# Performance work log

Hardware: AMD Instinct MI355X
Metric: run time of the kernel (lower is better)

Reference implementation:

```python
import jax, jax.numpy as jnp
import numpy as np

DIST_THRESHOLD = 0.1  # distance_threshold from __init__
NO_CODE_ID = -1


def setup_inputs() -> dict:
    key = jax.random.key(0)
    k1, k2 = jax.random.split(key)
    x = jax.random.normal(k1, (16, 4096, 64), dtype=jnp.float32)
    codes = jax.random.normal(k2, (4096, 64), dtype=jnp.float32)  # active codebook rows
    return {"x": x, "codes": codes}


def reference(x, codes):
    # Squared Euclidean distance (cdist ** 2) via the expansion
    x2 = jnp.sum(x * x, axis=-1, keepdims=True)            # [B, N, 1]
    c2 = jnp.sum(codes * codes, axis=-1)                    # [M]
    d2 = x2 + c2 - 2.0 * jnp.einsum("bnd,md->bnm", x, codes)  # [B, N, M]
    within = jnp.any(d2 <= DIST_THRESHOLD, axis=-1)         # [B, N]
    nn_ids = jnp.argmin(d2, axis=-1)                        # [B, N]
    return jnp.where(within, nn_ids, NO_CODE_ID)
```

## Files before the change

### kernel.cpp

```cpp
#include <hip/hip_runtime.h>
#include <stdint.h>

typedef float f32x4 __attribute__((ext_vector_type(4)));
typedef __bf16 bf16x8 __attribute__((ext_vector_type(8)));
typedef __bf16 bf16x4 __attribute__((ext_vector_type(4)));

#define NROWS 65536
#define NCODES 4096
#define NDIM 64
#define NSPLIT 4
#define STEPS 32
#define CBBYTEMASK 0x7FFFF
#define NCMASK 0xFFF


__device__ __forceinline__ void gld_lds16(const void* g, void* l) {
  __builtin_amdgcn_global_load_lds(
      (const __attribute__((address_space(1))) unsigned int*)g,
      (__attribute__((address_space(3))) unsigned int*)l, 16, 0, 0);
}

__global__ __launch_bounds__(256) void prep_codes_k(const float* __restrict__ codes,
                                                    float* __restrict__ nc2h,
                                                    __bf16* __restrict__ cb) {
  const int t = blockIdx.x * 256 + threadIdx.x;
  f32x4 v = *(const f32x4*)(codes + t * 4);
  bf16x4 o;
  float s = 0.f;
#pragma unroll
  for (int j = 0; j < 4; j++) {
    o[j] = (__bf16)v[j];
    s += v[j] * v[j];
  }
  *(bf16x4*)(cb + t * 4) = o;
  s += __shfl_xor(s, 1);
  s += __shfl_xor(s, 2);
  s += __shfl_xor(s, 4);
  s += __shfl_xor(s, 8);
  if ((threadIdx.x & 15) == 0) nc2h[t >> 4] = -0.5f * s;
}

__global__ __launch_bounds__(256, 4) void nn_main(const float* __restrict__ x,
                                                  const __bf16* __restrict__ cbv,
                                                  const float* __restrict__ nc2h,
                                                  float* __restrict__ tarr,
                                                  int* __restrict__ marr,
                                                  float* __restrict__ x2arr) {
  const int tid  = threadIdx.x;
  const int lane = tid & 63;
  const int w    = tid >> 6;
  const int col  = lane & 15;
  const int quad = lane >> 4;
  const int stripe = blockIdx.x & 3;
  const int rowgrp = blockIdx.x >> 2;
  const int rowbase = rowgrp * 256 + w * 64;
  const char* cbb = (const char*)cbv;

  __shared__ __align__(16) char stage[2][4096];

  bf16x8 a[4][2];
  float x2part[4];
#pragma unroll
  for (int rt = 0; rt < 4; rt++) {
    const float* xr = x + (rowbase + rt * 16 + col) * NDIM + quad * 8;
    float p = 0.f;
#pragma unroll
    for (int kc = 0; kc < 2; kc++) {
      f32x4 v0 = *(const f32x4*)(xr + kc * 32);
      f32x4 v1 = *(const f32x4*)(xr + kc * 32 + 4);
      bf16x8 af;
#pragma unroll
      for (int j = 0; j < 4; j++) {
        af[j]     = (__bf16)v0[j];
        af[j + 4] = (__bf16)v1[j];
        p += v0[j] * v0[j] + v1[j] * v1[j];
      }
      a[rt][kc] = af;
    }
    x2part[rt] = p;
  }
#pragma unroll
  for (int rt = 0; rt < 4; rt++) {
    float p = x2part[rt];
    p += __shfl_xor(p, 16);
    p += __shfl_xor(p, 32);
    x2part[rt] = p;
  }
  if (stripe == 0 && quad == 0) {
#pragma unroll
    for (int rt = 0; rt < 4; rt++) x2arr[rowbase + rt * 16 + col] = x2part[rt];
  }

  float bestT[4][4];
  int bestM[4][4];
#pragma unroll
  for (int rt = 0; rt < 4; rt++)
#pragma unroll
    for (int j = 0; j < 4; j++) {
      bestT[rt][j] = -3.0e38f;
      bestM[rt][j] = 0;
    }

  const uint32_t schunk = ((uint32_t)(tid * 16)) ^ ((((uint32_t)tid >> 3) & 7u) << 4);
  uint32_t sbyte = (uint32_t)stripe * 131072u + schunk;
  char* ldst0 = &stage[0][w * 1024];
  char* ldst1 = &stage[1][w * 1024];

  const uint32_t swz = ((uint32_t)(col & 7)) << 4;
  const uint32_t o00 = ((uint32_t)(col * 128 + quad * 16)) ^ swz;
  const uint32_t o01 = ((uint32_t)(col * 128 + 64 + quad * 16)) ^ swz;
  const uint32_t o10 = ((uint32_t)(2048 + col * 128 + quad * 16)) ^ swz;
  const uint32_t o11 = ((uint32_t)(2048 + col * 128 + 64 + quad * 16)) ^ swz;

  const int nb = stripe * 1024 + col;
  float nv0 = nc2h[nb];
  float nv1 = nc2h[nb + 16];

  gld_lds16(cbb + (sbyte & CBBYTEMASK), ldst0);
  sbyte += 4096;
  __syncthreads();

  int mi = stripe * 1024 + col;

#pragma unroll 1
  for (int s = 0; s < STEPS; s += 2) {
    gld_lds16(cbb + (sbyte & CBBYTEMASK), ldst1);
    sbyte += 4096;
    uint32_t nxt = (uint32_t)(nb + (s + 1) * 32);
    float nv0n = nc2h[nxt & NCMASK];
    float nv1n = nc2h[(nxt + 16) & NCMASK];
    {
      const char* sb = stage[0];
      bf16x8 b00 = *(const bf16x8*)(sb + o00);
      bf16x8 b01 = *(const bf16x8*)(sb + o01);
      bf16x8 b10 = *(const bf16x8*)(sb + o10);
      bf16x8 b11 = *(const bf16x8*)(sb + o11);
      f32x4 ci0 = {nv0, nv0, nv0, nv0};
      f32x4 ci1 = {nv1, nv1, nv1, nv1};
#pragma unroll
      for (int rt = 0; rt < 4; rt++) {
        f32x4 acc0 = __builtin_amdgcn_mfma_f32_16x16x32_bf16(a[rt][0], b00, ci0, 0, 0, 0);
        acc0 = __builtin_amdgcn_mfma_f32_16x16x32_bf16(a[rt][1], b01, acc0, 0, 0, 0);
        f32x4 acc1 = __builtin_amdgcn_mfma_f32_16x16x32_bf16(a[rt][0], b10, ci1, 0, 0, 0);
        acc1 = __builtin_amdgcn_mfma_f32_16x16x32_bf16(a[rt][1], b11, acc1, 0, 0, 0);
#pragma unroll
        for (int j = 0; j < 4; j++) {
          if (acc0[j] > bestT[rt][j]) { bestT[rt][j] = acc0[j]; bestM[rt][j] = mi; }
          if (acc1[j] > bestT[rt][j]) { bestT[rt][j] = acc1[j]; bestM[rt][j] = mi + 16; }
        }
      }
    }
    nv0 = nv0n; nv1 = nv1n;
    mi += 32;
    __syncthreads();

    gld_lds16(cbb + (sbyte & CBBYTEMASK), ldst0);
    sbyte += 4096;
    nxt = (uint32_t)(nb + (s + 2) * 32);
    nv0n = nc2h[nxt & NCMASK];
    nv1n = nc2h[(nxt + 16) & NCMASK];
    {
      const char* sb = stage[1];
      bf16x8 b00 = *(const bf16x8*)(sb + o00);
      bf16x8 b01 = *(const bf16x8*)(sb + o01);
      bf16x8 b10 = *(const bf16x8*)(sb + o10);
      bf16x8 b11 = *(const bf16x8*)(sb + o11);
      f32x4 ci0 = {nv0, nv0, nv0, nv0};
      f32x4 ci1 = {nv1, nv1, nv1, nv1};
#pragma unroll
      for (int rt = 0; rt < 4; rt++) {
        f32x4 acc0 = __builtin_amdgcn_mfma_f32_16x16x32_bf16(a[rt][0], b00, ci0, 0, 0, 0);
        acc0 = __builtin_amdgcn_mfma_f32_16x16x32_bf16(a[rt][1], b01, acc0, 0, 0, 0);
        f32x4 acc1 = __builtin_amdgcn_mfma_f32_16x16x32_bf16(a[rt][0], b10, ci1, 0, 0, 0);
        acc1 = __builtin_amdgcn_mfma_f32_16x16x32_bf16(a[rt][1], b11, acc1, 0, 0, 0);
#pragma unroll
        for (int j = 0; j < 4; j++) {
          if (acc0[j] > bestT[rt][j]) { bestT[rt][j] = acc0[j]; bestM[rt][j] = mi; }
          if (acc1[j] > bestT[rt][j]) { bestT[rt][j] = acc1[j]; bestM[rt][j] = mi + 16; }
        }
      }
    }
    nv0 = nv0n; nv1 = nv1n;
    mi += 32;
    __syncthreads();
  }

#pragma unroll
  for (int rt = 0; rt < 4; rt++) {
#pragma unroll
    for (int j = 0; j < 4; j++) {
      float bt = bestT[rt][j];
      int bm = bestM[rt][j];
#pragma unroll
      for (int off = 1; off < 16; off <<= 1) {
        float ot = __shfl_xor(bt, off);
        int om = __shfl_xor(bm, off);
        if (ot > bt || (ot == bt && om < bm)) {
          bt = ot;
          bm = om;
        }
      }
      if (col == 0) {
        const int row = rowbase + rt * 16 + quad * 4 + j;
        tarr[row * NSPLIT + stripe] = bt;
        marr[row * NSPLIT + stripe] = bm;
      }
    }
  }
}

__global__ __launch_bounds__(256) void nn_final(const float* __restrict__ tarr,
                                                const int* __restrict__ marr,
                                                const float* __restrict__ x2arr,
                                                int* __restrict__ out) {
  const int row = blockIdx.x * blockDim.x + threadIdx.x;
  if (row >= NROWS) return;
  float bt = tarr[row * NSPLIT];
  int bm = marr[row * NSPLIT];
#pragma unroll
  for (int s = 1; s < NSPLIT; s++) {
    float t = tarr[row * NSPLIT + s];
    int m = marr[row * NSPLIT + s];
    if (t > bt || (t == bt && m < bm)) {
      bt = t;
      bm = m;
    }
  }
  const float d2 = fmaf(-2.0f, bt, x2arr[row]);
  out[row] = (d2 <= 0.1f) ? bm : -1;
}

extern "C" void kernel_launch(void* const* d_in, const int* in_sizes, int n_in,
                              void* d_out, int out_size, void* d_ws, size_t ws_size,
                              hipStream_t stream) {
  const float* x = (const float*)d_in[0];
  const float* codes = (const float*)d_in[1];
  int* out = (int*)d_out;

  char* ws = (char*)d_ws;
  __bf16* cb = (__bf16*)ws;
  float* nc2h = (float*)(ws + 0x080000);
  float* tarr = (float*)(ws + 0x100000);
  int* marr = (int*)(ws + 0x200000);
  float* x2arr = (float*)(ws + 0x300000);

  prep_codes_k<<<256, 256, 0, stream>>>(codes, nc2h, cb);
  nn_main<<<1024, 256, 0, stream>>>(x, cb, nc2h, tarr, marr, x2arr);
  nn_final<<<256, 256, 0, stream>>>(tarr, marr, x2arr, out);
}
```

Measured before the change: 117.1 us.

## Batch codebook staging into 4-step phases and preload code norms into LDS

```diff
diff --git a/kernel.cpp b/kernel.cpp
--- a/kernel.cpp
+++ b/kernel.cpp
@@ -10,8 +10,8 @@
 #define NDIM 64
 #define NSPLIT 4
 #define STEPS 32
-#define CBBYTEMASK 0x7FFFF
-#define NCMASK 0xFFF
+#define SSTEP 4
+#define PHASES (STEPS / SSTEP)
 
 
 __device__ __forceinline__ void gld_lds16(const void* g, void* l) {
@@ -21,7 +21,7 @@
 }
 
 __global__ __launch_bounds__(256) void prep_codes_k(const float* __restrict__ codes,
-                                                    float* __restrict__ nc2h,
+                                                    float* __restrict__ nc2p,
                                                     __bf16* __restrict__ cb) {
   const int t = blockIdx.x * 256 + threadIdx.x;
   f32x4 v = *(const f32x4*)(codes + t * 4);
@@ -37,12 +37,17 @@
   s += __shfl_xor(s, 2);
   s += __shfl_xor(s, 4);
   s += __shfl_xor(s, 8);
-  if ((threadIdx.x & 15) == 0) nc2h[t >> 4] = -0.5f * s;
+  if ((threadIdx.x & 15) == 0) {
+    const int c = t >> 4;
+    const int pidx = (c >> 10) * 512 + ((c >> 5) & 31) * 16 + (c & 15);
+    const int half = (c >> 4) & 1;
+    nc2p[pidx * 2 + half] = -0.5f * s;
+  }
 }
 
 __global__ __launch_bounds__(256, 4) void nn_main(const float* __restrict__ x,
                                                   const __bf16* __restrict__ cbv,
-                                                  const float* __restrict__ nc2h,
+                                                  const float2* __restrict__ nc2p,
                                                   float* __restrict__ tarr,
                                                   int* __restrict__ marr,
                                                   float* __restrict__ x2arr) {
@@ -51,12 +56,20 @@
   const int w    = tid >> 6;
   const int col  = lane & 15;
   const int quad = lane >> 4;
-  const int stripe = blockIdx.x & 3;
-  const int rowgrp = blockIdx.x >> 2;
+  const int stripe = blockIdx.x >> 8;
+  const int rowgrp = blockIdx.x & 255;
   const int rowbase = rowgrp * 256 + w * 64;
   const char* cbb = (const char*)cbv;
 
-  __shared__ __align__(16) char stage[2][4096];
+  __shared__ __align__(16) char stage[2][SSTEP * 4096];
+  __shared__ __align__(8) float2 ncl[512];
+
+  const uint32_t schunk = ((uint32_t)(tid * 16)) ^ ((((uint32_t)tid >> 3) & 7u) << 4);
+  const char* srcbase = cbb + (uint32_t)stripe * 131072u + schunk;
+  gld_lds16((const char*)nc2p + stripe * 4096 + tid * 16, (char*)ncl + w * 1024);
+#pragma unroll
+  for (int i = 0; i < SSTEP; i++)
+    gld_lds16(srcbase + i * 4096, &stage[0][i * 4096 + w * 1024]);
 
   bf16x8 a[4][2];
   float x2part[4];
@@ -101,42 +114,37 @@
       bestM[rt][j] = 0;
     }
 
-  const uint32_t schunk = ((uint32_t)(tid * 16)) ^ ((((uint32_t)tid >> 3) & 7u) << 4);
-  uint32_t sbyte = (uint32_t)stripe * 131072u + schunk;
-  char* ldst0 = &stage[0][w * 1024];
-  char* ldst1 = &stage[1][w * 1024];
-
   const uint32_t swz = ((uint32_t)(col & 7)) << 4;
   const uint32_t o00 = ((uint32_t)(col * 128 + quad * 16)) ^ swz;
   const uint32_t o01 = ((uint32_t)(col * 128 + 64 + quad * 16)) ^ swz;
   const uint32_t o10 = ((uint32_t)(2048 + col * 128 + quad * 16)) ^ swz;
   const uint32_t o11 = ((uint32_t)(2048 + col * 128 + 64 + quad * 16)) ^ swz;
 
-  const int nb = stripe * 1024 + col;
-  float nv0 = nc2h[nb];
-  float nv1 = nc2h[nb + 16];
-
-  gld_lds16(cbb + (sbyte & CBBYTEMASK), ldst0);
-  sbyte += 4096;
+  const int mibase = stripe * 1024 + col;
+
   __syncthreads();
 
-  int mi = stripe * 1024 + col;
-
 #pragma unroll 1
-  for (int s = 0; s < STEPS; s += 2) {
-    gld_lds16(cbb + (sbyte & CBBYTEMASK), ldst1);
-    sbyte += 4096;
-    uint32_t nxt = (uint32_t)(nb + (s + 1) * 32);
-    float nv0n = nc2h[nxt & NCMASK];
-    float nv1n = nc2h[(nxt + 16) & NCMASK];
-    {
-      const char* sb = stage[0];
-      bf16x8 b00 = *(const bf16x8*)(sb + o00);
-      bf16x8 b01 = *(const bf16x8*)(sb + o01);
-      bf16x8 b10 = *(const bf16x8*)(sb + o10);
-      bf16x8 b11 = *(const bf16x8*)(sb + o11);
-      f32x4 ci0 = {nv0, nv0, nv0, nv0};
-      f32x4 ci1 = {nv1, nv1, nv1, nv1};
+  for (int p = 0; p < PHASES; ++p) {
+    if (p < PHASES - 1) {
+      const char* sp = srcbase + (p + 1) * (SSTEP * 4096);
+      char* dst = &stage[(p + 1) & 1][w * 1024];
+#pragma unroll
+      for (int i = 0; i < SSTEP; i++) gld_lds16(sp + i * 4096, dst + i * 4096);
+    }
+    const char* sb = stage[p & 1];
+#pragma unroll
+    for (int ss = 0; ss < SSTEP; ss++) {
+      const int s = p * SSTEP + ss;
+      const float2 nv = ncl[s * 16 + col];
+      bf16x8 b00 = *(const bf16x8*)(sb + ss * 4096 + o00);
+      bf16x8 b01 = *(const bf16x8*)(sb + ss * 4096 + o01);
+      bf16x8 b10 = *(const bf16x8*)(sb + ss * 4096 + o10);
+      bf16x8 b11 = *(const bf16x8*)(sb + ss * 4096 + o11);
+      f32x4 ci0 = {nv.x, nv.x, nv.x, nv.x};
+      f32x4 ci1 = {nv.y, nv.y, nv.y, nv.y};
+      const int mi0 = mibase + s * 32;
+      const int mi1 = mi0 + 16;
 #pragma unroll
       for (int rt = 0; rt < 4; rt++) {
         f32x4 acc0 = __builtin_amdgcn_mfma_f32_16x16x32_bf16(a[rt][0], b00, ci0, 0, 0, 0);
@@ -145,43 +153,11 @@
         acc1 = __builtin_amdgcn_mfma_f32_16x16x32_bf16(a[rt][1], b11, acc1, 0, 0, 0);
 #pragma unroll
         for (int j = 0; j < 4; j++) {
-          if (acc0[j] > bestT[rt][j]) { bestT[rt][j] = acc0[j]; bestM[rt][j] = mi; }
-          if (acc1[j] > bestT[rt][j]) { bestT[rt][j] = acc1[j]; bestM[rt][j] = mi + 16; }
+          if (acc0[j] > bestT[rt][j]) { bestT[rt][j] = acc0[j]; bestM[rt][j] = mi0; }
+          if (acc1[j] > bestT[rt][j]) { bestT[rt][j] = acc1[j]; bestM[rt][j] = mi1; }
         }
       }
     }
-    nv0 = nv0n; nv1 = nv1n;
-    mi += 32;
-    __syncthreads();
-
-    gld_lds16(cbb + (sbyte & CBBYTEMASK), ldst0);
-    sbyte += 4096;
-    nxt = (uint32_t)(nb + (s + 2) * 32);
-    nv0n = nc2h[nxt & NCMASK];
-    nv1n = nc2h[(nxt + 16) & NCMASK];
-    {
-      const char* sb = stage[1];
-      bf16x8 b00 = *(const bf16x8*)(sb + o00);
-      bf16x8 b01 = *(const bf16x8*)(sb + o01);
-      bf16x8 b10 = *(const bf16x8*)(sb + o10);
-      bf16x8 b11 = *(const bf16x8*)(sb + o11);
-      f32x4 ci0 = {nv0, nv0, nv0, nv0};
-      f32x4 ci1 = {nv1, nv1, nv1, nv1};
-#pragma unroll
-      for (int rt = 0; rt < 4; rt++) {
-        f32x4 acc0 = __builtin_amdgcn_mfma_f32_16x16x32_bf16(a[rt][0], b00, ci0, 0, 0, 0);
-        acc0 = __builtin_amdgcn_mfma_f32_16x16x32_bf16(a[rt][1], b01, acc0, 0, 0, 0);
-        f32x4 acc1 = __builtin_amdgcn_mfma_f32_16x16x32_bf16(a[rt][0], b10, ci1, 0, 0, 0);
-        acc1 = __builtin_amdgcn_mfma_f32_16x16x32_bf16(a[rt][1], b11, acc1, 0, 0, 0);
-#pragma unroll
-        for (int j = 0; j < 4; j++) {
-          if (acc0[j] > bestT[rt][j]) { bestT[rt][j] = acc0[j]; bestM[rt][j] = mi; }
-          if (acc1[j] > bestT[rt][j]) { bestT[rt][j] = acc1[j]; bestM[rt][j] = mi + 16; }
-        }
-      }
-    }
-    nv0 = nv0n; nv1 = nv1n;
-    mi += 32;
     __syncthreads();
   }
 
@@ -239,12 +215,12 @@
 
   char* ws = (char*)d_ws;
   __bf16* cb = (__bf16*)ws;
-  float* nc2h = (float*)(ws + 0x080000);
+  float* nc2p = (float*)(ws + 0x080000);
   float* tarr = (float*)(ws + 0x100000);
   int* marr = (int*)(ws + 0x200000);
   float* x2arr = (float*)(ws + 0x300000);
 
-  prep_codes_k<<<256, 256, 0, stream>>>(codes, nc2h, cb);
-  nn_main<<<1024, 256, 0, stream>>>(x, cb, nc2h, tarr, marr, x2arr);
+  prep_codes_k<<<256, 256, 0, stream>>>(codes, nc2p, cb);
+  nn_main<<<1024, 256, 0, stream>>>(x, cb, (const float2*)nc2p, tarr, marr, x2arr);
   nn_final<<<256, 256, 0, stream>>>(tarr, marr, x2arr, out);
 }
```

Measured after the change: 118.1 us. No clear change (+0.8%).
